# Performance work log

Measured on AMD Instinct MI355X. Metric: run time of the kernel, lower is better.

Reference implementation:

```python
import jax, jax.numpy as jnp
import numpy as np

K = 12
CHUNK = 1024
N_LAYERS = 4
WIDTH = 192
COND = 64
PE_DIM = 3 * 8 * 2 + 3  # 51
OUT_SCALE = 0.01
BIG = 1e9


def _build_knn(x, k=K, chunk=CHUNK):
    """Brute-force kNN, row-chunked like the TF double-chunked version.
    x: (N,3) float32 -> (N,k) int32 neighbor indices (self excluded)."""
    n = x.shape[0]
    x = x.astype(jnp.float32)
    x_sq = jnp.sum(x * x, axis=1)  # (N,)
    col_ids = jnp.arange(n, dtype=jnp.int32)
    starts = jnp.arange(0, n, chunk, dtype=jnp.int32)

    def one_chunk(start):
        xc = jax.lax.dynamic_slice(x, (start, 0), (chunk, 3))        # (chunk,3)
        sq_c = jax.lax.dynamic_slice(x_sq, (start,), (chunk,))       # (chunk,)
        d = sq_c[:, None] + x_sq[None, :] - 2.0 * (xc @ x.T)         # (chunk,N)
        d = jnp.maximum(d, 0.0)
        rows = start + jnp.arange(chunk, dtype=jnp.int32)
        d = d + jnp.where(rows[:, None] == col_ids[None, :], BIG, 0.0)  # exclude self
        _, idx = jax.lax.top_k(-d, k)                                 # smallest distances
        return idx.astype(jnp.int32)

    idx = jax.lax.map(one_chunk, starts)  # (n/chunk, chunk, k)
    return idx.reshape(n, k)


def _fourier(x, Bs):
    """concat_k [sin(xB_k), cos(xB_k)] + x  -> (N, PE_DIM)."""
    feats = []
    for B in Bs:
        xb = x @ B  # (N,8)
        feats.append(jnp.sin(xb))
        feats.append(jnp.cos(xb))
    feats.append(x)
    return jnp.concatenate(feats, axis=-1)


def setup_inputs() -> dict:
    key = jax.random.key(0)
    ks = jax.random.split(key, 16)
    n = 32768
    x = jax.random.normal(ks[0], (n, 3), dtype=jnp.float32)
    z = jax.random.normal(ks[1], (COND,), dtype=jnp.float32)
    sigmas = (1.0, 10.0, 50.0)
    B0 = jax.random.normal(ks[2], (3, 8), dtype=jnp.float32) * sigmas[0]
    B1 = jax.random.normal(ks[3], (3, 8), dtype=jnp.float32) * sigmas[1]
    B2 = jax.random.normal(ks[4], (3, 8), dtype=jnp.float32) * sigmas[2]
    in_total = PE_DIM + COND  # 115
    s = 0.05
    Wp = jax.random.normal(ks[5], (in_total, WIDTH), dtype=jnp.float32) * s
    bp = jnp.zeros((WIDTH,), dtype=jnp.float32)
    mix_dim = WIDTH + WIDTH + 6  # feat + agg + rel_feat
    Wl = jax.random.normal(ks[6], (N_LAYERS, mix_dim, WIDTH), dtype=jnp.float32) * s
    bl = jnp.zeros((N_LAYERS, WIDTH), dtype=jnp.float32)
    # FiLM: kernel ~zeros, gamma bias=ones, beta bias=zeros (perturbed slightly)
    Wg = jax.random.normal(ks[7], (N_LAYERS, COND, WIDTH), dtype=jnp.float32) * 0.01
    bg = jnp.ones((N_LAYERS, WIDTH), dtype=jnp.float32)
    Wb = jax.random.normal(ks[8], (N_LAYERS, COND, WIDTH), dtype=jnp.float32) * 0.01
    bb = jnp.zeros((N_LAYERS, WIDTH), dtype=jnp.float32)
    Wout = jax.random.normal(ks[9], (WIDTH, 3), dtype=jnp.float32) * s
    bout = jnp.zeros((3,), dtype=jnp.float32)
    return {"x": x, "z": z, "B0": B0, "B1": B1, "B2": B2,
            "Wp": Wp, "bp": bp, "Wl": Wl, "bl": bl,
            "Wg": Wg, "bg": bg, "Wb": Wb, "bb": bb,
            "Wout": Wout, "bout": bout}


def reference(x, z, B0, B1, B2, Wp, bp, Wl, bl, Wg, bg, Wb, bb, Wout, bout):
    n = x.shape[0]
    knn_idx = _build_knn(x)                     # (N,K) int32
    pe = _fourier(x, (B0, B1, B2))              # (N,51)
    zb = jnp.broadcast_to(z[None, :], (n, COND))
    feat = jnp.concatenate([pe, zb], axis=-1)   # (N,115)
    h = jax.nn.silu(feat @ Wp + bp)             # (N,WIDTH)
    # precompute relative-coordinate stats (same for all layers)
    nbr_coords = x[knn_idx]                     # (N,K,3)
    rel = nbr_coords - x[:, None, :]
    rel_feat = jnp.concatenate([rel.mean(axis=1), rel.std(axis=1)], axis=-1)  # (N,6)
    for li in range(N_LAYERS):
        nbr = h[knn_idx]                        # (N,K,WIDTH) gather
        agg = nbr.mean(axis=1)                  # (N,WIDTH)
        mix = jnp.concatenate([h, agg, rel_feat], axis=-1)  # (N,390)
        h = jax.nn.silu(mix @ Wl[li] + bl[li])
        gamma = z @ Wg[li] + bg[li]             # (WIDTH,)
        beta = z @ Wb[li] + bb[li]
        h = h * gamma[None, :] + beta[None, :]  # FiLM
    out = (h @ Wout + bout) * OUT_SCALE         # (N,3)
    return out
```

## Files before the change

kernel.cpp:

```cpp
#include <hip/hip_runtime.h>
#include <math.h>

#define WIDTH 192
#define KNN 12
#define G 64
#define NCELLS (G * G * G)
#define SMAX 8

#define CE(a, b) { double _lo = fmin(a, b); double _hi = fmax(a, b); a = _lo; b = _hi; }
#define INSERT12(key) { \
    b11 = fmin(b11, key); \
    CE(b10, b11); CE(b9, b10); CE(b8, b9); CE(b7, b8); CE(b6, b7); \
    CE(b5, b6);  CE(b4, b5); CE(b3, b4); CE(b2, b3); CE(b1, b2); CE(b0, b1); }
#define DECL12 double b0,b1,b2,b3,b4,b5,b6,b7,b8,b9,b10,b11
#define INIT12 { b0=__hiloint2double(0x7F7FFFFF,0);  b1=__hiloint2double(0x7F7FFFFF,1); \
    b2=__hiloint2double(0x7F7FFFFF,2);  b3=__hiloint2double(0x7F7FFFFF,3); \
    b4=__hiloint2double(0x7F7FFFFF,4);  b5=__hiloint2double(0x7F7FFFFF,5); \
    b6=__hiloint2double(0x7F7FFFFF,6);  b7=__hiloint2double(0x7F7FFFFF,7); \
    b8=__hiloint2double(0x7F7FFFFF,8);  b9=__hiloint2double(0x7F7FFFFF,9); \
    b10=__hiloint2double(0x7F7FFFFF,10); b11=__hiloint2double(0x7F7FFFFF,11); }

#define MERGE_STAGE(m) { \
    double pb11 = shflx_d(b11, m), pb10 = shflx_d(b10, m), pb9 = shflx_d(b9, m); \
    double pb8  = shflx_d(b8, m),  pb7  = shflx_d(b7, m),  pb6 = shflx_d(b6, m); \
    double pb5  = shflx_d(b5, m),  pb4  = shflx_d(b4, m),  pb3 = shflx_d(b3, m); \
    double pb2  = shflx_d(b2, m),  pb1  = shflx_d(b1, m),  pb0 = shflx_d(b0, m); \
    double c12 = pb3, c13 = pb2, c14 = pb1, c15 = pb0; \
    b4 = fmin(b4, pb11); b5 = fmin(b5, pb10); b6 = fmin(b6, pb9);  b7 = fmin(b7, pb8); \
    b8 = fmin(b8, pb7);  b9 = fmin(b9, pb6);  b10 = fmin(b10, pb5); b11 = fmin(b11, pb4); \
    CE(b0, b8);  CE(b1, b9);  CE(b2, b10); CE(b3, b11); \
    CE(b4, c12); CE(b5, c13); CE(b6, c14); CE(b7, c15); \
    CE(b0, b4);  CE(b1, b5);  CE(b2, b6);  CE(b3, b7); \
    CE(b8, c12); CE(b9, c13); CE(b10, c14); CE(b11, c15); \
    CE(b0, b2);  CE(b1, b3);  CE(b4, b6);  CE(b5, b7); \
    CE(b8, b10); CE(b9, b11); \
    CE(b0, b1);  CE(b2, b3);  CE(b4, b5);  CE(b6, b7); \
    CE(b8, b9);  CE(b10, b11); }

__device__ inline unsigned encf(float f) {
    unsigned u = __float_as_uint(f);
    return (u & 0x80000000u) ? ~u : (u | 0x80000000u);
}
__device__ inline float decf(unsigned u) {
    return (u & 0x80000000u) ? __uint_as_float(u & 0x7fffffffu) : __uint_as_float(~u);
}
__device__ inline int cellc(float v, float mn, float invh) {
    int c = (int)((v - mn) * invh);
    return min(max(c, 0), G - 1);
}
__device__ inline double shflx_d(double v, int m) {
    int lo = __shfl_xor(__double2loint(v), m, 64);
    int hi = __shfl_xor(__double2hiint(v), m, 64);
    return __hiloint2double(hi, lo);
}

__device__ inline float wave_union_d12(
    double b0, double b1, double b2, double b3, double b4, double b5,
    double b6, double b7, double b8, double b9, double b10, double b11)
{
#pragma unroll
    for (int m = 1; m <= 32; m <<= 1) MERGE_STAGE(m)
    return __int_as_float(__double2hiint(b11));
}

__global__ __launch_bounds__(256) void prep_kernel(
    const float4* __restrict__ sorted, const float* __restrict__ B0,
    const float* __restrict__ B1, const float* __restrict__ B2,
    float* __restrict__ pe, int n)
{
    int i = blockIdx.x * 256 + threadIdx.x;
    float4 q = sorted[i];
    float x0 = q.x, x1 = q.y, x2 = q.z;
    const float* Bm[3] = {B0, B1, B2};
    float* pr = pe + (size_t)i * 64;
#pragma unroll
    for (int m = 0; m < 3; ++m) {
        const float* B = Bm[m];
#pragma unroll
        for (int k = 0; k < 8; ++k) {
            float arg = x0 * B[k] + x1 * B[8 + k] + x2 * B[16 + k];
            pr[m * 16 + k]     = sinf(arg);
            pr[m * 16 + 8 + k] = cosf(arg);
        }
    }
    pr[48] = x0; pr[49] = x1; pr[50] = x2;
#pragma unroll
    for (int c = 51; c < 64; ++c) pr[c] = 0.0f;
}

__global__ __launch_bounds__(256) void precompute_kernel(
    const float* __restrict__ z, const float* __restrict__ Wp, const float* __restrict__ bp,
    const float* __restrict__ Wg, const float* __restrict__ bg,
    const float* __restrict__ Wb, const float* __restrict__ bb,
    float* __restrict__ bias0, float* __restrict__ gammaB, float* __restrict__ betaB)
{
    __shared__ float zs[64];
    int t = threadIdx.x;
    if (t < 64) zs[t] = z[t];
    __syncthreads();
    if (t < WIDTH) {
        float acc = bp[t];
        for (int k = 0; k < 64; ++k) acc += zs[k] * Wp[(51 + k) * WIDTH + t];
        bias0[t] = acc;
        for (int l = 0; l < 4; ++l) {
            float g = bg[l * WIDTH + t];
            float b = bb[l * WIDTH + t];
            for (int k = 0; k < 64; ++k) {
                g += zs[k] * Wg[(l * 64 + k) * WIDTH + t];
                b += zs[k] * Wb[(l * 64 + k) * WIDTH + t];
            }
            gammaB[l * WIDTH + t] = g;
            betaB[l * WIDTH + t] = b;
        }
    }
}

__global__ __launch_bounds__(64) void init_bbox_kernel(unsigned* __restrict__ bb)
{
    int t = threadIdx.x;
    if (t < 3) bb[t] = 0xFFFFFFFFu;
    else if (t < 6) bb[t] = 0u;
}

__global__ __launch_bounds__(256) void bbox_kernel(
    const float* __restrict__ x, unsigned* __restrict__ bb, int n)
{
    int i = blockIdx.x * 256 + threadIdx.x;
    unsigned emin[3], emax[3];
#pragma unroll
    for (int a = 0; a < 3; ++a) { unsigned e = encf(x[i * 3 + a]); emin[a] = e; emax[a] = e; }
#pragma unroll
    for (int o = 32; o; o >>= 1) {
#pragma unroll
        for (int a = 0; a < 3; ++a) {
            emin[a] = min(emin[a], (unsigned)__shfl_xor((int)emin[a], o, 64));
            emax[a] = max(emax[a], (unsigned)__shfl_xor((int)emax[a], o, 64));
        }
    }
    if ((threadIdx.x & 63) == 0) {
#pragma unroll
        for (int a = 0; a < 3; ++a) {
            atomicMin(&bb[a], emin[a]);
            atomicMax(&bb[3 + a], emax[a]);
        }
    }
}

__global__ __launch_bounds__(256) void hist_kernel(
    const float* __restrict__ x, const unsigned* __restrict__ bb,
    unsigned* __restrict__ counts, unsigned long long* __restrict__ rowmask, int n)
{
    int i = blockIdx.x * 256 + threadIdx.x;
    float mnx = decf(bb[0]), mny = decf(bb[1]), mnz = decf(bb[2]);
    float ivx = (float)G / (decf(bb[3]) - mnx);
    float ivy = (float)G / (decf(bb[4]) - mny);
    float ivz = (float)G / (decf(bb[5]) - mnz);
    int cx = cellc(x[i * 3 + 0], mnx, ivx);
    int cy = cellc(x[i * 3 + 1], mny, ivy);
    int cz = cellc(x[i * 3 + 2], mnz, ivz);
    atomicAdd(&counts[(cz * G + cy) * G + cx], 1u);
    atomicOr(&rowmask[cz * G + cy], 1ull << cx);
}

__global__ __launch_bounds__(256) void scan1_kernel(
    const unsigned* __restrict__ counts, unsigned* __restrict__ offs,
    unsigned* __restrict__ bsums)
{
    __shared__ unsigned s[256];
    int b = blockIdx.x, t = threadIdx.x;
    unsigned base = (unsigned)b * 1024 + t * 4;
    unsigned v[4], sum = 0;
#pragma unroll
    for (int k = 0; k < 4; ++k) { v[k] = counts[base + k]; sum += v[k]; }
    s[t] = sum; __syncthreads();
    for (int off = 1; off < 256; off <<= 1) {
        unsigned xv = (t >= off) ? s[t - off] : 0u;
        __syncthreads();
        s[t] += xv;
        __syncthreads();
    }
    unsigned excl = s[t] - sum;
    if (t == 255) bsums[b] = s[255];
    unsigned run = excl;
#pragma unroll
    for (int k = 0; k < 4; ++k) { offs[base + k] = run; run += v[k]; }
}

__global__ __launch_bounds__(256) void scan2_kernel(unsigned* __restrict__ bsums)
{
    __shared__ unsigned s[256];
    int t = threadIdx.x;
    unsigned v = bsums[t];
    s[t] = v; __syncthreads();
    for (int off = 1; off < 256; off <<= 1) {
        unsigned xv = (t >= off) ? s[t - off] : 0u;
        __syncthreads();
        s[t] += xv;
        __syncthreads();
    }
    bsums[t] = s[t] - v;
}

__global__ __launch_bounds__(256) void scan3_kernel(
    unsigned* __restrict__ offs, const unsigned* __restrict__ bsums,
    unsigned* __restrict__ cursors, int n)
{
    int b = blockIdx.x, t = threadIdx.x;
    unsigned add = bsums[b];
    unsigned base = (unsigned)b * 1024 + t * 4;
#pragma unroll
    for (int k = 0; k < 4; ++k) {
        unsigned v = offs[base + k] + add;
        offs[base + k] = v;
        cursors[base + k] = v;
    }
    if (b == 255 && t == 255) offs[NCELLS] = (unsigned)n;
}

__global__ __launch_bounds__(256) void scatter_kernel(
    const float* __restrict__ x, const unsigned* __restrict__ bb,
    unsigned* __restrict__ cursors, float4* __restrict__ sorted,
    unsigned* __restrict__ inv, int n)
{
    int i = blockIdx.x * 256 + threadIdx.x;
    float mnx = decf(bb[0]), mny = decf(bb[1]), mnz = decf(bb[2]);
    float ivx = (float)G / (decf(bb[3]) - mnx);
    float ivy = (float)G / (decf(bb[4]) - mny);
    float ivz = (float)G / (decf(bb[5]) - mnz);
    float x0 = x[i * 3 + 0], x1 = x[i * 3 + 1], x2 = x[i * 3 + 2];
    int cx = cellc(x0, mnx, ivx);
    int cy = cellc(x1, mny, ivy);
    int cz = cellc(x2, mnz, ivz);
    unsigned pos = atomicAdd(&cursors[(cz * G + cy) * G + cx], 1u);
    sorted[pos] = make_float4(x0, x1, x2, __int_as_float(i));
    inv[i] = pos;
}

__global__ __launch_bounds__(256) void knn_grid_kernel(
    const float4* __restrict__ sorted, const unsigned* __restrict__ offs,
    const unsigned long long* __restrict__ rowmask,
    const unsigned* __restrict__ bb, const float* __restrict__ x,
    const unsigned* __restrict__ inv,
    unsigned short* __restrict__ knn, float* __restrict__ relf, int n)
{
    const int tid = threadIdx.x;
    const int l = tid & 63;
    const int nb = gridDim.x;
    const int b = blockIdx.x;
    const int fb = (b & 1) ? (nb - 1 - (b >> 1)) : (b >> 1);
    const int p = fb * 4 + (tid >> 6);

    float mnx = decf(bb[0]), mny = decf(bb[1]), mnz = decf(bb[2]);
    float mxx = decf(bb[3]), mxy = decf(bb[4]), mxz = decf(bb[5]);
    float hx = (mxx - mnx) / G, hy = (mxy - mny) / G, hz = (mxz - mnz) / G;
    float ivx = (float)G / (mxx - mnx);
    float ivy = (float)G / (mxy - mny);
    float ivz = (float)G / (mxz - mnz);

    float4 q = sorted[p];
    float xi = q.x, yi = q.y, zi = q.z;
    int iorig = __float_as_int(q.w);
    float sqi = fmaf(zi, zi, fmaf(yi, yi, xi * xi));
    int cx = cellc(xi, mnx, ivx), cy = cellc(yi, mny, ivy), cz = cellc(zi, mnz, ivz);
    float fx = (xi - mnx) - cx * hx;
    float fy = (yi - mny) - cy * hy;
    float fz = (zi - mnz) - cz * hz;

    DECL12; INIT12;
    float worst = 3.402823466e+38f;
    float worst_g = 3.402823466e+38f;

    auto waveMinWorst = [&]() -> float {
        float wm = worst;
        wm = fminf(wm, __shfl_xor(wm, 1, 64));
        wm = fminf(wm, __shfl_xor(wm, 2, 64));
        wm = fminf(wm, __shfl_xor(wm, 4, 64));
        wm = fminf(wm, __shfl_xor(wm, 8, 64));
        wm = fminf(wm, __shfl_xor(wm, 16, 64));
        wm = fminf(wm, __shfl_xor(wm, 32, 64));
        return wm;
    };

    auto lane12Bound = [&]() -> float {
        float v = __int_as_float(__double2hiint(b0));
#pragma unroll
        for (int k = 2; k <= 64; k <<= 1) {
#pragma unroll
            for (int j = k >> 1; j >= 1; j >>= 1) {
                float pv = __shfl_xor(v, j, 64);
                bool dir = ((l & k) == 0);
                bool lower = ((l & j) == 0);
                float mn = fminf(v, pv), mx = fmaxf(v, pv);
                v = (lower == dir) ? mn : mx;
            }
        }
        return __shfl(v, 11, 64);
    };

    auto scanRange = [&](int c0, int c1) {
        unsigned j0 = offs[c0], j1 = offs[c1 + 1];
        if (j0 >= j1) return;
        float4 c = sorted[j0];
        for (unsigned t = j0; t < j1; ++t) {
            unsigned tn = (t + 1 < j1) ? t + 1 : t;
            float4 nx = sorted[tn];
            float sqj = fmaf(c.z, c.z, fmaf(c.y, c.y, c.x * c.x));
            float dot = fmaf(zi, c.z, fmaf(yi, c.y, xi * c.x));
            float d = fmaf(-2.0f, dot, sqi + sqj);
            int jg = __float_as_int(c.w);
            if (d <= fminf(worst, worst_g) && jg != iorig) {
                d = fmaxf(d, 0.0f);
                double key = __hiloint2double(__float_as_int(d), jg);
                INSERT12(key);
                worst = __int_as_float(__double2hiint(b11));
            }
            c = nx;
        }
    };

    auto scanStrided = [&](int c0, int c1, int sub, int step) {
        unsigned j0 = offs[c0], j1 = offs[c1 + 1];
        for (unsigned t = j0 + sub; t < j1; t += step) {
            float4 c = sorted[t];
            float sqj = fmaf(c.z, c.z, fmaf(c.y, c.y, c.x * c.x));
            float dot = fmaf(zi, c.z, fmaf(yi, c.y, xi * c.x));
            float d = fmaf(-2.0f, dot, sqi + sqj);
            int jg = __float_as_int(c.w);
            if (d <= fminf(worst, worst_g) && jg != iorig) {
                d = fmaxf(d, 0.0f);
                double key = __hiloint2double(__float_as_int(d), jg);
                INSERT12(key);
                worst = __int_as_float(__double2hiint(b11));
            }
        }
    };

    auto doRow = [&](int s, int dz, int dy, int sub, int step) {
        int zz = cz + dz, yy = cy + dy;
        if (zz < 0 || zz >= G || yy < 0 || yy >= G) return;
        int row = zz * G + yy;
        unsigned long long rm = rowmask[row];
        if (rm == 0ull) return;
        int rb = row * G;
        int adz = dz < 0 ? -dz : dz, ady = dy < 0 ? -dy : dy;
        if (adz == s || ady == s) {
            int x0 = max(cx - s, 0), x1 = min(cx + s, G - 1);
            unsigned long long msk =
                ((x1 == 63) ? ~0ull : ((1ull << (x1 + 1)) - 1ull)) &
                ~((1ull << x0) - 1ull);
            unsigned long long mm = rm & msk;
            if (mm) {
                int c0 = __ffsll((unsigned long long)mm) - 1;
                int c1 = 63 - __clzll((long long)mm);
                if (step == 1) scanRange(rb + c0, rb + c1);
                else           scanStrided(rb + c0, rb + c1, sub, step);
            }
        } else {
            int xm = cx - s, xp = cx + s;
            if (xm >= 0 && ((rm >> xm) & 1ull)) {
                if (step == 1) scanRange(rb + xm, rb + xm);
                else           scanStrided(rb + xm, rb + xm, sub, step);
            }
            if (xp < G && ((rm >> xp) & 1ull)) {
                if (step == 1) scanRange(rb + xp, rb + xp);
                else           scanStrided(rb + xp, rb + xp, sub, step);
            }
        }
    };

    bool done = false;
    for (int s = 0; s <= SMAX; ++s) {
        if (s > 0) {
            float bx = (s - 1) * hx + fminf(fx, hx - fx);
            float by = (s - 1) * hy + fminf(fy, hy - fy);
            float bz = (s - 1) * hz + fminf(fz, hz - fz);
            float bnd = fminf(bx, fminf(by, bz));
            float bnd2 = bnd * bnd;
            worst_g = fminf(worst_g, waveMinWorst());
            if (bnd2 > worst_g + 1e-4f) { done = true; break; }
            worst_g = fminf(worst_g, lane12Bound());
            if (bnd2 > worst_g + 1e-4f) { done = true; break; }
            if (s >= 2) {
                worst_g = fminf(worst_g,
                    wave_union_d12(b0,b1,b2,b3,b4,b5,b6,b7,b8,b9,b10,b11));
                if (bnd2 > worst_g + 1e-4f) { done = true; break; }
            }
        }
        if (s == 0) {
            int row = cz * G + cy;
            if ((rowmask[row] >> cx) & 1ull) {
                int rb = row * G;
                scanStrided(rb + cx, rb + cx, l, 64);
            }
        } else {
            int w2 = 2 * s + 1;
            int nrows = w2 * w2;
            int lpr = 64 / nrows;
            if (lpr > 1) {
                int r = l / lpr, sub = l - r * lpr;
                if (r < nrows) {
                    int dz = r / w2 - s, dy = r - (r / w2) * w2 - s;
                    doRow(s, dz, dy, sub, lpr);
                }
            } else {
                float rcp = 1.0f / (float)w2;
                for (int r = l; r < nrows; r += 64) {
                    int qd = (int)((float)r * rcp);
                    int rem = r - qd * w2;
                    if (rem < 0) { qd--; rem += w2; }
                    else if (rem >= w2) { qd++; rem -= w2; }
                    doRow(s, qd - s, rem - s, 0, 1);
                }
            }
        }
    }
    if (!done) {
        float bx = SMAX * hx + fminf(fx, hx - fx);
        float by = SMAX * hy + fminf(fy, hy - fy);
        float bz = SMAX * hz + fminf(fz, hz - fz);
        float bnd = fminf(bx, fminf(by, bz));
        float bnd2 = bnd * bnd;
        worst_g = fminf(worst_g, waveMinWorst());
        if (bnd2 > worst_g + 1e-4f) done = true;
        if (!done) {
            worst_g = fminf(worst_g, lane12Bound());
            if (bnd2 > worst_g + 1e-4f) done = true;
        }
        if (!done) {
            worst_g = fminf(worst_g,
                wave_union_d12(b0,b1,b2,b3,b4,b5,b6,b7,b8,b9,b10,b11));
            if (bnd2 > worst_g + 1e-4f) done = true;
        }
    }
    if (!done) {
        INIT12;
        worst = 3.402823466e+38f;
        for (int base = 0; base < n; base += 512) {
            float4 cc[8];
#pragma unroll
            for (int r = 0; r < 8; ++r) cc[r] = sorted[base + l + r * 64];
#pragma unroll
            for (int r = 0; r < 8; ++r) {
                float4 c = cc[r];
                float sqj = fmaf(c.z, c.z, fmaf(c.y, c.y, c.x * c.x));
                float dot = fmaf(zi, c.z, fmaf(yi, c.y, xi * c.x));
                float d = fmaf(-2.0f, dot, sqi + sqj);
                int jg = __float_as_int(c.w);
                if (d <= fminf(worst, worst_g) && jg != iorig) {
                    d = fmaxf(d, 0.0f);
                    double key = __hiloint2double(__float_as_int(d), jg);
                    INSERT12(key);
                    worst = __int_as_float(__double2hiint(b11));
                }
            }
        }
    }

#pragma unroll
    for (int m = 1; m <= 32; m <<= 1) MERGE_STAGE(m)

    if (l == 0) {
        int idx[KNN];
        idx[0]=__double2loint(b0);  idx[1]=__double2loint(b1);  idx[2]=__double2loint(b2);
        idx[3]=__double2loint(b3);  idx[4]=__double2loint(b4);  idx[5]=__double2loint(b5);
        idx[6]=__double2loint(b6);  idx[7]=__double2loint(b7);  idx[8]=__double2loint(b8);
        idx[9]=__double2loint(b9);  idx[10]=__double2loint(b10); idx[11]=__double2loint(b11);

        float rx[KNN], ry[KNN], rz[KNN];
        float sx = 0.f, sy = 0.f, sz = 0.f;
#pragma unroll
        for (int s = 0; s < KNN; ++s) {
            int j = idx[s];
            knn[(size_t)p * KNN + s] = (unsigned short)inv[j];
            rx[s] = x[(size_t)j * 3 + 0] - xi;
            ry[s] = x[(size_t)j * 3 + 1] - yi;
            rz[s] = x[(size_t)j * 3 + 2] - zi;
            sx += rx[s]; sy += ry[s]; sz += rz[s];
        }
        float mx = sx / 12.0f, my = sy / 12.0f, mz = sz / 12.0f;
        float vx = 0.f, vy = 0.f, vz = 0.f;
#pragma unroll
        for (int s = 0; s < KNN; ++s) {
            float dx = rx[s] - mx, dy = ry[s] - my, dz = rz[s] - mz;
            vx += dx * dx; vy += dy * dy; vz += dz * dz;
        }
        float* rr = relf + (size_t)p * 8;
        rr[0] = mx; rr[1] = my; rr[2] = mz;
        rr[3] = sqrtf(vx / 12.0f); rr[4] = sqrtf(vy / 12.0f); rr[5] = sqrtf(vz / 12.0f);
        rr[6] = 0.0f; rr[7] = 0.0f;
    }
}

template <bool LAYER>
__global__ __launch_bounds__(256) void gemm_silu_kernel(
    const float* __restrict__ A0, const unsigned short* __restrict__ knnp,
    const float* __restrict__ Rel,
    const float* __restrict__ W, const float* __restrict__ bias,
    const float* __restrict__ gamma, const float* __restrict__ beta,
    float* __restrict__ out)
{
    __shared__ float As[16][68];
    __shared__ float Bs[16][196];
    const int tid = threadIdx.x;
    const int ty = tid >> 4, tx = tid & 15;
    const int m0 = blockIdx.x * 64;
    const int arow = tid >> 2, akoff = (tid & 3) * 4;
    const int bk = tid >> 4,  bc = (tid & 15) * 12;

    float acc[4][12] = {};
    const int NCH = LAYER ? 24 : 4;

    auto loadA = [&](int ch) -> float4 {
        int k0 = ch * 16;
        if (!LAYER) {
            return *(const float4*)&A0[(size_t)(m0 + arow) * 64 + k0 + akoff];
        } else if (k0 < 192) {
            return *(const float4*)&A0[(size_t)(m0 + arow) * 192 + k0 + akoff];
        } else {
            int c4 = (k0 - 192 + akoff) >> 2;
            const unsigned short* kn = knnp + (size_t)(m0 + arow) * KNN;
            const float4* h4 = (const float4*)A0;
            float4 s = make_float4(0.f, 0.f, 0.f, 0.f);
#pragma unroll
            for (int j = 0; j < KNN; ++j) {
                float4 v = h4[(size_t)kn[j] * 48 + c4];
                s.x += v.x; s.y += v.y; s.z += v.z; s.w += v.w;
            }
            const float r = 1.0f / 12.0f;
            return make_float4(s.x * r, s.y * r, s.z * r, s.w * r);
        }
    };

    float4 ra = loadA(0);
    const float* wr0 = &W[(size_t)bk * 192 + bc];
    float4 rb0 = *(const float4*)&wr0[0];
    float4 rb1 = *(const float4*)&wr0[4];
    float4 rb2 = *(const float4*)&wr0[8];

    for (int ch = 0; ch < NCH; ++ch) {
        As[akoff + 0][arow] = ra.x; As[akoff + 1][arow] = ra.y;
        As[akoff + 2][arow] = ra.z; As[akoff + 3][arow] = ra.w;
        *(float4*)&Bs[bk][bc + 0] = rb0;
        *(float4*)&Bs[bk][bc + 4] = rb1;
        *(float4*)&Bs[bk][bc + 8] = rb2;
        __syncthreads();
        if (ch + 1 < NCH) {
            ra = loadA(ch + 1);
            const float* wr = &W[(size_t)((ch + 1) * 16 + bk) * 192 + bc];
            rb0 = *(const float4*)&wr[0];
            rb1 = *(const float4*)&wr[4];
            rb2 = *(const float4*)&wr[8];
        }
#pragma unroll
        for (int k = 0; k < 16; ++k) {
            float4 a0 = *(const float4*)&As[k][ty * 4];
            float av[4] = {a0.x, a0.y, a0.z, a0.w};
            float4 q0 = *(const float4*)&Bs[k][tx * 12 + 0];
            float4 q1 = *(const float4*)&Bs[k][tx * 12 + 4];
            float4 q2 = *(const float4*)&Bs[k][tx * 12 + 8];
            float bv[12] = {q0.x, q0.y, q0.z, q0.w, q1.x, q1.y, q1.z, q1.w,
                            q2.x, q2.y, q2.z, q2.w};
#pragma unroll
            for (int a = 0; a < 4; ++a)
#pragma unroll
                for (int bcol = 0; bcol < 12; ++bcol)
                    acc[a][bcol] = fmaf(av[a], bv[bcol], acc[a][bcol]);
        }
        __syncthreads();
    }

    if (LAYER) {
        {
            int row = tid >> 2, cp = (tid & 3) * 2;
            float2 v = *(const float2*)&Rel[(size_t)(m0 + row) * 8 + cp];
            As[cp + 0][row] = v.x; As[cp + 1][row] = v.y;
        }
        {
            int k2 = tid >> 4, c = (tid & 15) * 12;
            if (k2 < 8) {
                int gk = 384 + k2; if (gk > 389) gk = 389;
                const float* wr = &W[(size_t)gk * 192 + c];
                *(float4*)&Bs[k2][c + 0] = *(const float4*)&wr[0];
                *(float4*)&Bs[k2][c + 4] = *(const float4*)&wr[4];
                *(float4*)&Bs[k2][c + 8] = *(const float4*)&wr[8];
            }
        }
        __syncthreads();
#pragma unroll
        for (int k = 0; k < 8; ++k) {
            float4 a0 = *(const float4*)&As[k][ty * 4];
            float av[4] = {a0.x, a0.y, a0.z, a0.w};
            float4 q0 = *(const float4*)&Bs[k][tx * 12 + 0];
            float4 q1 = *(const float4*)&Bs[k][tx * 12 + 4];
            float4 q2 = *(const float4*)&Bs[k][tx * 12 + 8];
            float bv[12] = {q0.x, q0.y, q0.z, q0.w, q1.x, q1.y, q1.z, q1.w,
                            q2.x, q2.y, q2.z, q2.w};
#pragma unroll
            for (int a = 0; a < 4; ++a)
#pragma unroll
                for (int bcol = 0; bcol < 12; ++bcol)
                    acc[a][bcol] = fmaf(av[a], bv[bcol], acc[a][bcol]);
        }
        __syncthreads();
    }

#pragma unroll
    for (int a = 0; a < 4; ++a) {
        int gi = m0 + ty * 4 + a;
        float res[12];
#pragma unroll
        for (int bcol = 0; bcol < 12; ++bcol) {
            int gc = tx * 12 + bcol;
            float v = acc[a][bcol] + bias[gc];
            float s = 1.0f / (1.0f + expf(-v));
            v = v * s;
            if (LAYER) v = v * gamma[gc] + beta[gc];
            res[bcol] = v;
        }
        float* orow = &out[(size_t)gi * 192 + tx * 12];
        *(float4*)&orow[0] = make_float4(res[0], res[1], res[2], res[3]);
        *(float4*)&orow[4] = make_float4(res[4], res[5], res[6], res[7]);
        *(float4*)&orow[8] = make_float4(res[8], res[9], res[10], res[11]);
    }
}

__global__ __launch_bounds__(256) void out_kernel(
    const float4* __restrict__ h4, const float4* __restrict__ sorted,
    const float* __restrict__ Wout, const float* __restrict__ bout,
    float* __restrict__ out, int n)
{
    __shared__ float w[576];
    int t = threadIdx.x;
    for (int e = t; e < 576; e += 256) w[e] = Wout[e];
    __syncthreads();
    int i = blockIdx.x * 256 + t;
    float a0 = 0.f, a1 = 0.f, a2 = 0.f;
    for (int k4 = 0; k4 < 48; ++k4) {
        float4 hv = h4[(size_t)i * 48 + k4];
        int k = k4 * 4;
        a0 = fmaf(hv.x, w[k * 3 + 0], a0); a1 = fmaf(hv.x, w[k * 3 + 1], a1); a2 = fmaf(hv.x, w[k * 3 + 2], a2);
        a0 = fmaf(hv.y, w[k * 3 + 3], a0); a1 = fmaf(hv.y, w[k * 3 + 4], a1); a2 = fmaf(hv.y, w[k * 3 + 5], a2);
        a0 = fmaf(hv.z, w[k * 3 + 6], a0); a1 = fmaf(hv.z, w[k * 3 + 7], a1); a2 = fmaf(hv.z, w[k * 3 + 8], a2);
        a0 = fmaf(hv.w, w[k * 3 + 9], a0); a1 = fmaf(hv.w, w[k * 3 + 10], a1); a2 = fmaf(hv.w, w[k * 3 + 11], a2);
    }
    int iorig = __float_as_int(sorted[i].w);
    out[(size_t)iorig * 3 + 0] = (a0 + bout[0]) * 0.01f;
    out[(size_t)iorig * 3 + 1] = (a1 + bout[1]) * 0.01f;
    out[(size_t)iorig * 3 + 2] = (a2 + bout[2]) * 0.01f;
}

extern "C" void kernel_launch(void* const* d_in, const int* in_sizes, int n_in,
                              void* d_out, int out_size, void* d_ws, size_t ws_size,
                              hipStream_t stream)
{
    const float* x    = (const float*)d_in[0];
    const float* z    = (const float*)d_in[1];
    const float* B0   = (const float*)d_in[2];
    const float* B1   = (const float*)d_in[3];
    const float* B2   = (const float*)d_in[4];
    const float* Wp   = (const float*)d_in[5];
    const float* bp   = (const float*)d_in[6];
    const float* Wl   = (const float*)d_in[7];
    const float* bl   = (const float*)d_in[8];
    const float* Wg   = (const float*)d_in[9];
    const float* bg   = (const float*)d_in[10];
    const float* Wb   = (const float*)d_in[11];
    const float* bb   = (const float*)d_in[12];
    const float* Wout = (const float*)d_in[13];
    const float* bout = (const float*)d_in[14];

    int n = in_sizes[0] / 3;

    float* ws = (float*)d_ws;
    float* bias0  = ws;
    float* gammaB = ws + 192;
    float* betaB  = ws + 960;
    size_t off = 1728;
    unsigned short* knn = (unsigned short*)(ws + off);  off += (size_t)n * 6;
    float* relf = ws + off;                off += (size_t)n * 8;
    float4* sorted = (float4*)(ws + off);  off += (size_t)n * 4;
    float* hA   = ws + off;                off += (size_t)n * 192;
    float* hB   = ws + off;                off += (size_t)n * 192;

    unsigned* bbx     = (unsigned*)hA;
    unsigned* counts  = bbx + 8;
    unsigned* offsA   = counts + NCELLS;
    unsigned* cursors = offsA + NCELLS + 1;
    unsigned* bsums   = cursors + NCELLS;
    size_t gu = 8 + (size_t)NCELLS * 3 + 1 + 256;
    gu = (gu + 1) & ~(size_t)1;
    unsigned long long* rowmask = (unsigned long long*)((unsigned*)hA + gu);
    gu += (size_t)G * G * 2;
    unsigned* inv = (unsigned*)hA + gu;
    float* pe = hB;

    init_bbox_kernel<<<1, 64, 0, stream>>>(bbx);
    hipMemsetAsync(counts, 0, (size_t)NCELLS * 4, stream);
    hipMemsetAsync(rowmask, 0, (size_t)G * G * 8, stream);
    precompute_kernel<<<1, 256, 0, stream>>>(z, Wp, bp, Wg, bg, Wb, bb,
                                             bias0, gammaB, betaB);
    bbox_kernel<<<n / 256, 256, 0, stream>>>(x, bbx, n);
    hist_kernel<<<n / 256, 256, 0, stream>>>(x, bbx, counts, rowmask, n);
    scan1_kernel<<<NCELLS / 1024, 256, 0, stream>>>(counts, offsA, bsums);
    scan2_kernel<<<1, 256, 0, stream>>>(bsums);
    scan3_kernel<<<NCELLS / 1024, 256, 0, stream>>>(offsA, bsums, cursors, n);
    scatter_kernel<<<n / 256, 256, 0, stream>>>(x, bbx, cursors, sorted, inv, n);
    prep_kernel<<<n / 256, 256, 0, stream>>>(sorted, B0, B1, B2, pe, n);
    knn_grid_kernel<<<n / 4, 256, 0, stream>>>(sorted, offsA, rowmask, bbx, x,
                                               inv, knn, relf, n);

    gemm_silu_kernel<false><<<n / 64, 256, 0, stream>>>(
        pe, nullptr, nullptr, Wp, bias0, nullptr, nullptr, hA);

    float* hcur = hA;
    float* hnxt = hB;
    for (int li = 0; li < 4; ++li) {
        gemm_silu_kernel<true><<<n / 64, 256, 0, stream>>>(
            hcur, knn, relf,
            Wl + (size_t)li * 390 * 192, bl + (size_t)li * 192,
            gammaB + (size_t)li * 192, betaB + (size_t)li * 192, hnxt);
        float* t = hcur; hcur = hnxt; hnxt = t;
    }

    out_kernel<<<n / 256, 256, 0, stream>>>((const float4*)hcur, sorted,
                                            Wout, bout, (float*)d_out, n);
}
```

Baseline: 767.9 us.

## Use persistent atomic work queue for kNN waves and gate bound checks

The kNN kernel now runs a fixed grid of persistent blocks, and each wave pulls query points from a global atomic counter instead of being assigned one point per wave statically. This is meant to balance the uneven per-point search cost. The costly cross-lane bound computations (lane12Bound, wave_union_d12) are now skipped until enough candidates exist across the wave. Separately, the layer GEMM loads each row's 12 neighbor indices once into packed registers instead of reloading them for every K chunk. The changes add an atomic per point and a counter that must be reset with a memset.

```diff
diff --git a/kernel.cpp b/kernel.cpp
--- a/kernel.cpp
+++ b/kernel.cpp
@@ -240,15 +240,11 @@
     const float4* __restrict__ sorted, const unsigned* __restrict__ offs,
     const unsigned long long* __restrict__ rowmask,
     const unsigned* __restrict__ bb, const float* __restrict__ x,
-    const unsigned* __restrict__ inv,
+    const unsigned* __restrict__ inv, unsigned* __restrict__ wq,
     unsigned short* __restrict__ knn, float* __restrict__ relf, int n)
 {
     const int tid = threadIdx.x;
     const int l = tid & 63;
-    const int nb = gridDim.x;
-    const int b = blockIdx.x;
-    const int fb = (b & 1) ? (nb - 1 - (b >> 1)) : (b >> 1);
-    const int p = fb * 4 + (tid >> 6);
 
     float mnx = decf(bb[0]), mny = decf(bb[1]), mnz = decf(bb[2]);
     float mxx = decf(bb[3]), mxy = decf(bb[4]), mxz = decf(bb[5]);
@@ -257,191 +253,62 @@
     float ivy = (float)G / (mxy - mny);
     float ivz = (float)G / (mxz - mnz);
 
-    float4 q = sorted[p];
-    float xi = q.x, yi = q.y, zi = q.z;
-    int iorig = __float_as_int(q.w);
-    float sqi = fmaf(zi, zi, fmaf(yi, yi, xi * xi));
-    int cx = cellc(xi, mnx, ivx), cy = cellc(yi, mny, ivy), cz = cellc(zi, mnz, ivz);
-    float fx = (xi - mnx) - cx * hx;
-    float fy = (yi - mny) - cy * hy;
-    float fz = (zi - mnz) - cz * hz;
-
-    DECL12; INIT12;
-    float worst = 3.402823466e+38f;
-    float worst_g = 3.402823466e+38f;
-
-    auto waveMinWorst = [&]() -> float {
-        float wm = worst;
-        wm = fminf(wm, __shfl_xor(wm, 1, 64));
-        wm = fminf(wm, __shfl_xor(wm, 2, 64));
-        wm = fminf(wm, __shfl_xor(wm, 4, 64));
-        wm = fminf(wm, __shfl_xor(wm, 8, 64));
-        wm = fminf(wm, __shfl_xor(wm, 16, 64));
-        wm = fminf(wm, __shfl_xor(wm, 32, 64));
-        return wm;
-    };
-
-    auto lane12Bound = [&]() -> float {
-        float v = __int_as_float(__double2hiint(b0));
-#pragma unroll
-        for (int k = 2; k <= 64; k <<= 1) {
-#pragma unroll
-            for (int j = k >> 1; j >= 1; j >>= 1) {
-                float pv = __shfl_xor(v, j, 64);
-                bool dir = ((l & k) == 0);
-                bool lower = ((l & j) == 0);
-                float mn = fminf(v, pv), mx = fmaxf(v, pv);
-                v = (lower == dir) ? mn : mx;
-            }
-        }
-        return __shfl(v, 11, 64);
-    };
-
-    auto scanRange = [&](int c0, int c1) {
-        unsigned j0 = offs[c0], j1 = offs[c1 + 1];
-        if (j0 >= j1) return;
-        float4 c = sorted[j0];
-        for (unsigned t = j0; t < j1; ++t) {
-            unsigned tn = (t + 1 < j1) ? t + 1 : t;
-            float4 nx = sorted[tn];
-            float sqj = fmaf(c.z, c.z, fmaf(c.y, c.y, c.x * c.x));
-            float dot = fmaf(zi, c.z, fmaf(yi, c.y, xi * c.x));
-            float d = fmaf(-2.0f, dot, sqi + sqj);
-            int jg = __float_as_int(c.w);
-            if (d <= fminf(worst, worst_g) && jg != iorig) {
-                d = fmaxf(d, 0.0f);
-                double key = __hiloint2double(__float_as_int(d), jg);
-                INSERT12(key);
-                worst = __int_as_float(__double2hiint(b11));
-            }
-            c = nx;
-        }
-    };
-
-    auto scanStrided = [&](int c0, int c1, int sub, int step) {
-        unsigned j0 = offs[c0], j1 = offs[c1 + 1];
-        for (unsigned t = j0 + sub; t < j1; t += step) {
-            float4 c = sorted[t];
-            float sqj = fmaf(c.z, c.z, fmaf(c.y, c.y, c.x * c.x));
-            float dot = fmaf(zi, c.z, fmaf(yi, c.y, xi * c.x));
-            float d = fmaf(-2.0f, dot, sqi + sqj);
-            int jg = __float_as_int(c.w);
-            if (d <= fminf(worst, worst_g) && jg != iorig) {
-                d = fmaxf(d, 0.0f);
-                double key = __hiloint2double(__float_as_int(d), jg);
-                INSERT12(key);
-                worst = __int_as_float(__double2hiint(b11));
-            }
-        }
-    };
-
-    auto doRow = [&](int s, int dz, int dy, int sub, int step) {
-        int zz = cz + dz, yy = cy + dy;
-        if (zz < 0 || zz >= G || yy < 0 || yy >= G) return;
-        int row = zz * G + yy;
-        unsigned long long rm = rowmask[row];
-        if (rm == 0ull) return;
-        int rb = row * G;
-        int adz = dz < 0 ? -dz : dz, ady = dy < 0 ? -dy : dy;
-        if (adz == s || ady == s) {
-            int x0 = max(cx - s, 0), x1 = min(cx + s, G - 1);
-            unsigned long long msk =
-                ((x1 == 63) ? ~0ull : ((1ull << (x1 + 1)) - 1ull)) &
-                ~((1ull << x0) - 1ull);
-            unsigned long long mm = rm & msk;
-            if (mm) {
-                int c0 = __ffsll((unsigned long long)mm) - 1;
-                int c1 = 63 - __clzll((long long)mm);
-                if (step == 1) scanRange(rb + c0, rb + c1);
-                else           scanStrided(rb + c0, rb + c1, sub, step);
-            }
-        } else {
-            int xm = cx - s, xp = cx + s;
-            if (xm >= 0 && ((rm >> xm) & 1ull)) {
-                if (step == 1) scanRange(rb + xm, rb + xm);
-                else           scanStrided(rb + xm, rb + xm, sub, step);
-            }
-            if (xp < G && ((rm >> xp) & 1ull)) {
-                if (step == 1) scanRange(rb + xp, rb + xp);
-                else           scanStrided(rb + xp, rb + xp, sub, step);
-            }
-        }
-    };
-
-    bool done = false;
-    for (int s = 0; s <= SMAX; ++s) {
-        if (s > 0) {
-            float bx = (s - 1) * hx + fminf(fx, hx - fx);
-            float by = (s - 1) * hy + fminf(fy, hy - fy);
-            float bz = (s - 1) * hz + fminf(fz, hz - fz);
-            float bnd = fminf(bx, fminf(by, bz));
-            float bnd2 = bnd * bnd;
-            worst_g = fminf(worst_g, waveMinWorst());
-            if (bnd2 > worst_g + 1e-4f) { done = true; break; }
-            worst_g = fminf(worst_g, lane12Bound());
-            if (bnd2 > worst_g + 1e-4f) { done = true; break; }
-            if (s >= 2) {
-                worst_g = fminf(worst_g,
-                    wave_union_d12(b0,b1,b2,b3,b4,b5,b6,b7,b8,b9,b10,b11));
-                if (bnd2 > worst_g + 1e-4f) { done = true; break; }
-            }
-        }
-        if (s == 0) {
-            int row = cz * G + cy;
-            if ((rowmask[row] >> cx) & 1ull) {
-                int rb = row * G;
-                scanStrided(rb + cx, rb + cx, l, 64);
-            }
-        } else {
-            int w2 = 2 * s + 1;
-            int nrows = w2 * w2;
-            int lpr = 64 / nrows;
-            if (lpr > 1) {
-                int r = l / lpr, sub = l - r * lpr;
-                if (r < nrows) {
-                    int dz = r / w2 - s, dy = r - (r / w2) * w2 - s;
-                    doRow(s, dz, dy, sub, lpr);
-                }
-            } else {
-                float rcp = 1.0f / (float)w2;
-                for (int r = l; r < nrows; r += 64) {
-                    int qd = (int)((float)r * rcp);
-                    int rem = r - qd * w2;
-                    if (rem < 0) { qd--; rem += w2; }
-                    else if (rem >= w2) { qd++; rem -= w2; }
-                    doRow(s, qd - s, rem - s, 0, 1);
-                }
-            }
-        }
-    }
-    if (!done) {
-        float bx = SMAX * hx + fminf(fx, hx - fx);
-        float by = SMAX * hy + fminf(fy, hy - fy);
-        float bz = SMAX * hz + fminf(fz, hz - fz);
-        float bnd = fminf(bx, fminf(by, bz));
-        float bnd2 = bnd * bnd;
-        worst_g = fminf(worst_g, waveMinWorst());
-        if (bnd2 > worst_g + 1e-4f) done = true;
-        if (!done) {
-            worst_g = fminf(worst_g, lane12Bound());
-            if (bnd2 > worst_g + 1e-4f) done = true;
-        }
-        if (!done) {
-            worst_g = fminf(worst_g,
-                wave_union_d12(b0,b1,b2,b3,b4,b5,b6,b7,b8,b9,b10,b11));
-            if (bnd2 > worst_g + 1e-4f) done = true;
-        }
-    }
-    if (!done) {
-        INIT12;
-        worst = 3.402823466e+38f;
-        for (int base = 0; base < n; base += 512) {
-            float4 cc[8];
-#pragma unroll
-            for (int r = 0; r < 8; ++r) cc[r] = sorted[base + l + r * 64];
-#pragma unroll
-            for (int r = 0; r < 8; ++r) {
-                float4 c = cc[r];
+    for (;;) {
+        unsigned tk;
+        if (l == 0) tk = atomicAdd(wq, 1u);
+        tk = (unsigned)__shfl((int)tk, 0, 64);
+        if (tk >= (unsigned)n) break;
+        const int p = (tk & 1u) ? (n - 1 - (int)(tk >> 1)) : (int)(tk >> 1);
+
+        float4 q = sorted[p];
+        float xi = q.x, yi = q.y, zi = q.z;
+        int iorig = __float_as_int(q.w);
+        float sqi = fmaf(zi, zi, fmaf(yi, yi, xi * xi));
+        int cx = cellc(xi, mnx, ivx), cy = cellc(yi, mny, ivy), cz = cellc(zi, mnz, ivz);
+        float fx = (xi - mnx) - cx * hx;
+        float fy = (yi - mny) - cy * hy;
+        float fz = (zi - mnz) - cz * hz;
+
+        DECL12; INIT12;
+        float worst = 3.402823466e+38f;
+        float worst_g = 3.402823466e+38f;
+        int nc = 0;
+        bool have12 = false;
+
+        auto waveMinWorst = [&]() -> float {
+            float wm = worst;
+            wm = fminf(wm, __shfl_xor(wm, 1, 64));
+            wm = fminf(wm, __shfl_xor(wm, 2, 64));
+            wm = fminf(wm, __shfl_xor(wm, 4, 64));
+            wm = fminf(wm, __shfl_xor(wm, 8, 64));
+            wm = fminf(wm, __shfl_xor(wm, 16, 64));
+            wm = fminf(wm, __shfl_xor(wm, 32, 64));
+            return wm;
+        };
+
+        auto lane12Bound = [&]() -> float {
+            float v = __int_as_float(__double2hiint(b0));
+#pragma unroll
+            for (int k = 2; k <= 64; k <<= 1) {
+#pragma unroll
+                for (int j = k >> 1; j >= 1; j >>= 1) {
+                    float pv = __shfl_xor(v, j, 64);
+                    bool dir = ((l & k) == 0);
+                    bool lower = ((l & j) == 0);
+                    float mn = fminf(v, pv), mx = fmaxf(v, pv);
+                    v = (lower == dir) ? mn : mx;
+                }
+            }
+            return __shfl(v, 11, 64);
+        };
+
+        auto scanRange = [&](int c0, int c1) {
+            unsigned j0 = offs[c0], j1 = offs[c1 + 1];
+            if (j0 >= j1) return;
+            float4 c = sorted[j0];
+            for (unsigned t = j0; t < j1; ++t) {
+                unsigned tn = (t + 1 < j1) ? t + 1 : t;
+                float4 nx = sorted[tn];
                 float sqj = fmaf(c.z, c.z, fmaf(c.y, c.y, c.x * c.x));
                 float dot = fmaf(zi, c.z, fmaf(yi, c.y, xi * c.x));
                 float d = fmaf(-2.0f, dot, sqi + sqj);
@@ -451,43 +318,207 @@
                     double key = __hiloint2double(__float_as_int(d), jg);
                     INSERT12(key);
                     worst = __int_as_float(__double2hiint(b11));
-                }
-            }
-        }
-    }
-
-#pragma unroll
-    for (int m = 1; m <= 32; m <<= 1) MERGE_STAGE(m)
-
-    if (l == 0) {
-        int idx[KNN];
-        idx[0]=__double2loint(b0);  idx[1]=__double2loint(b1);  idx[2]=__double2loint(b2);
-        idx[3]=__double2loint(b3);  idx[4]=__double2loint(b4);  idx[5]=__double2loint(b5);
-        idx[6]=__double2loint(b6);  idx[7]=__double2loint(b7);  idx[8]=__double2loint(b8);
-        idx[9]=__double2loint(b9);  idx[10]=__double2loint(b10); idx[11]=__double2loint(b11);
-
-        float rx[KNN], ry[KNN], rz[KNN];
-        float sx = 0.f, sy = 0.f, sz = 0.f;
-#pragma unroll
-        for (int s = 0; s < KNN; ++s) {
-            int j = idx[s];
-            knn[(size_t)p * KNN + s] = (unsigned short)inv[j];
-            rx[s] = x[(size_t)j * 3 + 0] - xi;
-            ry[s] = x[(size_t)j * 3 + 1] - yi;
-            rz[s] = x[(size_t)j * 3 + 2] - zi;
-            sx += rx[s]; sy += ry[s]; sz += rz[s];
-        }
-        float mx = sx / 12.0f, my = sy / 12.0f, mz = sz / 12.0f;
-        float vx = 0.f, vy = 0.f, vz = 0.f;
-#pragma unroll
-        for (int s = 0; s < KNN; ++s) {
-            float dx = rx[s] - mx, dy = ry[s] - my, dz = rz[s] - mz;
-            vx += dx * dx; vy += dy * dy; vz += dz * dz;
-        }
-        float* rr = relf + (size_t)p * 8;
-        rr[0] = mx; rr[1] = my; rr[2] = mz;
-        rr[3] = sqrtf(vx / 12.0f); rr[4] = sqrtf(vy / 12.0f); rr[5] = sqrtf(vz / 12.0f);
-        rr[6] = 0.0f; rr[7] = 0.0f;
+                    ++nc;
+                }
+                c = nx;
+            }
+        };
+
+        auto scanStrided = [&](int c0, int c1, int sub, int step) {
+            unsigned j0 = offs[c0], j1 = offs[c1 + 1];
+            for (unsigned t = j0 + sub; t < j1; t += step) {
+                float4 c = sorted[t];
+                float sqj = fmaf(c.z, c.z, fmaf(c.y, c.y, c.x * c.x));
+                float dot = fmaf(zi, c.z, fmaf(yi, c.y, xi * c.x));
+                float d = fmaf(-2.0f, dot, sqi + sqj);
+                int jg = __float_as_int(c.w);
+                if (d <= fminf(worst, worst_g) && jg != iorig) {
+                    d = fmaxf(d, 0.0f);
+                    double key = __hiloint2double(__float_as_int(d), jg);
+                    INSERT12(key);
+                    worst = __int_as_float(__double2hiint(b11));
+                    ++nc;
+                }
+            }
+        };
+
+        auto doRow = [&](int s, int dz, int dy, int sub, int step) {
+            int zz = cz + dz, yy = cy + dy;
+            if (zz < 0 || zz >= G || yy < 0 || yy >= G) return;
+            int row = zz * G + yy;
+            unsigned long long rm = rowmask[row];
+            if (rm == 0ull) return;
+            int rb = row * G;
+            int adz = dz < 0 ? -dz : dz, ady = dy < 0 ? -dy : dy;
+            if (adz == s || ady == s) {
+                int x0 = max(cx - s, 0), x1 = min(cx + s, G - 1);
+                unsigned long long msk =
+                    ((x1 == 63) ? ~0ull : ((1ull << (x1 + 1)) - 1ull)) &
+                    ~((1ull << x0) - 1ull);
+                unsigned long long mm = rm & msk;
+                if (mm) {
+                    int c0 = __ffsll((unsigned long long)mm) - 1;
+                    int c1 = 63 - __clzll((long long)mm);
+                    if (step == 1) scanRange(rb + c0, rb + c1);
+                    else           scanStrided(rb + c0, rb + c1, sub, step);
+                }
+            } else {
+                int xm = cx - s, xp = cx + s;
+                if (xm >= 0 && ((rm >> xm) & 1ull)) {
+                    if (step == 1) scanRange(rb + xm, rb + xm);
+                    else           scanStrided(rb + xm, rb + xm, sub, step);
+                }
+                if (xp < G && ((rm >> xp) & 1ull)) {
+                    if (step == 1) scanRange(rb + xp, rb + xp);
+                    else           scanStrided(rb + xp, rb + xp, sub, step);
+                }
+            }
+        };
+
+        auto check12 = [&]() {
+            if (!have12) {
+                int ns = nc;
+#pragma unroll
+                for (int o = 1; o <= 32; o <<= 1) ns += __shfl_xor(ns, o, 64);
+                have12 = (ns >= 12);
+            }
+        };
+
+        bool done = false;
+        for (int s = 0; s <= SMAX; ++s) {
+            if (s > 0) {
+                float bx = (s - 1) * hx + fminf(fx, hx - fx);
+                float by = (s - 1) * hy + fminf(fy, hy - fy);
+                float bz = (s - 1) * hz + fminf(fz, hz - fz);
+                float bnd = fminf(bx, fminf(by, bz));
+                float bnd2 = bnd * bnd;
+                worst_g = fminf(worst_g, waveMinWorst());
+                if (bnd2 > worst_g + 1e-4f) { done = true; break; }
+                unsigned long long anyb =
+                    __ballot(__double2hiint(b0) != 0x7F7FFFFF);
+                if (__popcll(anyb) >= 12) {
+                    worst_g = fminf(worst_g, lane12Bound());
+                    if (bnd2 > worst_g + 1e-4f) { done = true; break; }
+                }
+                if (s >= 2) {
+                    check12();
+                    if (have12) {
+                        worst_g = fminf(worst_g,
+                            wave_union_d12(b0,b1,b2,b3,b4,b5,b6,b7,b8,b9,b10,b11));
+                        if (bnd2 > worst_g + 1e-4f) { done = true; break; }
+                    }
+                }
+            }
+            if (s == 0) {
+                int row = cz * G + cy;
+                if ((rowmask[row] >> cx) & 1ull) {
+                    int rb = row * G;
+                    scanStrided(rb + cx, rb + cx, l, 64);
+                }
+            } else {
+                int w2 = 2 * s + 1;
+                int nrows = w2 * w2;
+                int lpr = 64 / nrows;
+                if (lpr > 1) {
+                    int r = l / lpr, sub = l - r * lpr;
+                    if (r < nrows) {
+                        int dz = r / w2 - s, dy = r - (r / w2) * w2 - s;
+                        doRow(s, dz, dy, sub, lpr);
+                    }
+                } else {
+                    float rcp = 1.0f / (float)w2;
+                    for (int r = l; r < nrows; r += 64) {
+                        int qd = (int)((float)r * rcp);
+                        int rem = r - qd * w2;
+                        if (rem < 0) { qd--; rem += w2; }
+                        else if (rem >= w2) { qd++; rem -= w2; }
+                        doRow(s, qd - s, rem - s, 0, 1);
+                    }
+                }
+            }
+        }
+        if (!done) {
+            float bx = SMAX * hx + fminf(fx, hx - fx);
+            float by = SMAX * hy + fminf(fy, hy - fy);
+            float bz = SMAX * hz + fminf(fz, hz - fz);
+            float bnd = fminf(bx, fminf(by, bz));
+            float bnd2 = bnd * bnd;
+            worst_g = fminf(worst_g, waveMinWorst());
+            if (bnd2 > worst_g + 1e-4f) done = true;
+            if (!done) {
+                unsigned long long anyb =
+                    __ballot(__double2hiint(b0) != 0x7F7FFFFF);
+                if (__popcll(anyb) >= 12) {
+                    worst_g = fminf(worst_g, lane12Bound());
+                    if (bnd2 > worst_g + 1e-4f) done = true;
+                }
+            }
+            if (!done) {
+                check12();
+                if (have12) {
+                    worst_g = fminf(worst_g,
+                        wave_union_d12(b0,b1,b2,b3,b4,b5,b6,b7,b8,b9,b10,b11));
+                    if (bnd2 > worst_g + 1e-4f) done = true;
+                }
+            }
+        }
+        if (!done) {
+            INIT12;
+            worst = 3.402823466e+38f;
+            for (int base = 0; base < n; base += 512) {
+                float4 cc[8];
+#pragma unroll
+                for (int r = 0; r < 8; ++r) cc[r] = sorted[base + l + r * 64];
+#pragma unroll
+                for (int r = 0; r < 8; ++r) {
+                    float4 c = cc[r];
+                    float sqj = fmaf(c.z, c.z, fmaf(c.y, c.y, c.x * c.x));
+                    float dot = fmaf(zi, c.z, fmaf(yi, c.y, xi * c.x));
+                    float d = fmaf(-2.0f, dot, sqi + sqj);
+                    int jg = __float_as_int(c.w);
+                    if (d <= fminf(worst, worst_g) && jg != iorig) {
+                        d = fmaxf(d, 0.0f);
+                        double key = __hiloint2double(__float_as_int(d), jg);
+                        INSERT12(key);
+                        worst = __int_as_float(__double2hiint(b11));
+                    }
+                }
+            }
+        }
+
+#pragma unroll
+        for (int m = 1; m <= 32; m <<= 1) MERGE_STAGE(m)
+
+        if (l == 0) {
+            int idx[KNN];
+            idx[0]=__double2loint(b0);  idx[1]=__double2loint(b1);  idx[2]=__double2loint(b2);
+            idx[3]=__double2loint(b3);  idx[4]=__double2loint(b4);  idx[5]=__double2loint(b5);
+            idx[6]=__double2loint(b6);  idx[7]=__double2loint(b7);  idx[8]=__double2loint(b8);
+            idx[9]=__double2loint(b9);  idx[10]=__double2loint(b10); idx[11]=__double2loint(b11);
+
+            float rx[KNN], ry[KNN], rz[KNN];
+            float sx = 0.f, sy = 0.f, sz = 0.f;
+#pragma unroll
+            for (int s = 0; s < KNN; ++s) {
+                int j = idx[s];
+                knn[(size_t)p * KNN + s] = (unsigned short)inv[j];
+                rx[s] = x[(size_t)j * 3 + 0] - xi;
+                ry[s] = x[(size_t)j * 3 + 1] - yi;
+                rz[s] = x[(size_t)j * 3 + 2] - zi;
+                sx += rx[s]; sy += ry[s]; sz += rz[s];
+            }
+            float mx = sx / 12.0f, my = sy / 12.0f, mz = sz / 12.0f;
+            float vx = 0.f, vy = 0.f, vz = 0.f;
+#pragma unroll
+            for (int s = 0; s < KNN; ++s) {
+                float dx = rx[s] - mx, dy = ry[s] - my, dz = rz[s] - mz;
+                vx += dx * dx; vy += dy * dy; vz += dz * dz;
+            }
+            float* rr = relf + (size_t)p * 8;
+            rr[0] = mx; rr[1] = my; rr[2] = mz;
+            rr[3] = sqrtf(vx / 12.0f); rr[4] = sqrtf(vy / 12.0f); rr[5] = sqrtf(vz / 12.0f);
+            rr[6] = 0.0f; rr[7] = 0.0f;
+        }
     }
 }
 
@@ -509,6 +540,13 @@
 
     float acc[4][12] = {};
     const int NCH = LAYER ? 24 : 4;
+
+    unsigned kf[6] = {0, 0, 0, 0, 0, 0};
+    if (LAYER) {
+        const unsigned* kp = (const unsigned*)(knnp + (size_t)(m0 + arow) * KNN);
+#pragma unroll
+        for (int w = 0; w < 6; ++w) kf[w] = kp[w];
+    }
 
     auto loadA = [&](int ch) -> float4 {
         int k0 = ch * 16;
@@ -518,12 +556,12 @@
             return *(const float4*)&A0[(size_t)(m0 + arow) * 192 + k0 + akoff];
         } else {
             int c4 = (k0 - 192 + akoff) >> 2;
-            const unsigned short* kn = knnp + (size_t)(m0 + arow) * KNN;
             const float4* h4 = (const float4*)A0;
             float4 s = make_float4(0.f, 0.f, 0.f, 0.f);
 #pragma unroll
             for (int j = 0; j < KNN; ++j) {
-                float4 v = h4[(size_t)kn[j] * 48 + c4];
+                unsigned idx = (j & 1) ? (kf[j >> 1] >> 16) : (kf[j >> 1] & 0xFFFFu);
+                float4 v = h4[(size_t)idx * 48 + c4];
                 s.x += v.x; s.y += v.y; s.z += v.z; s.w += v.w;
             }
             const float r = 1.0f / 12.0f;
@@ -692,11 +730,13 @@
     unsigned long long* rowmask = (unsigned long long*)((unsigned*)hA + gu);
     gu += (size_t)G * G * 2;
     unsigned* inv = (unsigned*)hA + gu;
+    unsigned* wq  = inv + n;
     float* pe = hB;
 
     init_bbox_kernel<<<1, 64, 0, stream>>>(bbx);
     hipMemsetAsync(counts, 0, (size_t)NCELLS * 4, stream);
     hipMemsetAsync(rowmask, 0, (size_t)G * G * 8, stream);
+    hipMemsetAsync(wq, 0, 4, stream);
     precompute_kernel<<<1, 256, 0, stream>>>(z, Wp, bp, Wg, bg, Wb, bb,
                                              bias0, gammaB, betaB);
     bbox_kernel<<<n / 256, 256, 0, stream>>>(x, bbx, n);
@@ -706,8 +746,8 @@
     scan3_kernel<<<NCELLS / 1024, 256, 0, stream>>>(offsA, bsums, cursors, n);
     scatter_kernel<<<n / 256, 256, 0, stream>>>(x, bbx, cursors, sorted, inv, n);
     prep_kernel<<<n / 256, 256, 0, stream>>>(sorted, B0, B1, B2, pe, n);
-    knn_grid_kernel<<<n / 4, 256, 0, stream>>>(sorted, offsA, rowmask, bbx, x,
-                                               inv, knn, relf, n);
+    knn_grid_kernel<<<2048, 256, 0, stream>>>(sorted, offsA, rowmask, bbx, x,
+                                              inv, wq, knn, relf, n);
 
     gemm_silu_kernel<false><<<n / 64, 256, 0, stream>>>(
         pe, nullptr, nullptr, Wp, bias0, nullptr, nullptr, hA);
```

After: 1.058 ms. 1.38x slower.
